# Kernel tuning notes

Measured on AMD Instinct MI355X. Metric: run time of the kernel, lower is better.

Reference implementation:

```python
import jax, jax.numpy as jnp
import numpy as np

B, N, D, H, O = 20000, 32, 128, 256, 128
ATT_SLOPE = 0.01   # nn.LeakyReLU() default inside self.att
ALPHA = 0.2        # leakyrelu slope for attention scores


def _lrelu(v, slope):
    return jnp.where(v > 0, v, slope * v)


def setup_inputs() -> dict:
    key = jax.random.key(0)
    ks = jax.random.split(key, 6)
    x = jax.random.normal(ks[0], (B, D), dtype=jnp.float32)
    neibs = jax.random.normal(ks[1], (B * N, D), dtype=jnp.float32)
    # torch Linear weight is [out,in]; we store transposed [in,out] for x @ W
    W_att = jax.random.normal(ks[2], (D, H), dtype=jnp.float32) / np.sqrt(D)
    W_fcx = jax.random.normal(ks[3], (D, O), dtype=jnp.float32) / np.sqrt(D)
    W_fcn = jax.random.normal(ks[4], (D, O), dtype=jnp.float32) / np.sqrt(D)
    a = jax.random.normal(ks[5], (2 * H, 1), dtype=jnp.float32) * (1.414 * np.sqrt(6.0 / (2 * H + 1)))
    return {"x": x, "neibs": neibs, "W_att": W_att, "W_fcx": W_fcx, "W_fcn": W_fcn, "a": a}


def reference(x, neibs, W_att, W_fcx, W_fcn, a):
    b = x.shape[0]
    n = neibs.shape[0] // b
    # self.att = Linear(no bias) + LeakyReLU(default 0.01)
    x_att = _lrelu(x @ W_att, ATT_SLOPE)                       # [B,H]
    neib_att = _lrelu(neibs @ W_att, ATT_SLOPE).reshape(b, n, -1)  # [B,N,H]
    # cat([x_att.repeat, neib_att]) @ a  ==  x_att @ a[:H] + neib_att @ a[H:]
    h = W_att.shape[1]
    e = _lrelu(x_att @ a[:h, 0] + neib_att @ a[h:, 0][..., None] if False else
               (x_att @ a[:h, 0])[:, None] + jnp.einsum('bnh,h->bn', neib_att, a[h:, 0]), ALPHA)  # [B,N]
    attention = jax.nn.softmax(e, axis=1)                      # softmax over neighbors
    # dropout skipped (eval mode / training=False)
    agg_neib = jnp.einsum('bnd,bn->bd', neibs.reshape(b, n, -1), attention)  # [B,D]
    out = jnp.concatenate([x @ W_fcx, agg_neib @ W_fcn], axis=1)  # combine_fn = cat dim=1
    out = jax.nn.relu(out)                                     # activation
    return out
```

## Files before the change

### kernel.cpp

```cpp
#include <hip/hip_runtime.h>
#include <hip/hip_bf16.h>


#define BB 20000
#define NN 32
#define DD 128
#define HH 256
#define OO 128
#define MB 4
#define ROWS 144
#define AG0 132

typedef __bf16 bf16x8 __attribute__((ext_vector_type(8)));
typedef __bf16 bf16x4 __attribute__((ext_vector_type(4)));
typedef float f32x4 __attribute__((ext_vector_type(4)));

template<int CTRL>
__device__ __forceinline__ float dpp_add(float v) {
    int r = __builtin_amdgcn_update_dpp(0, __builtin_bit_cast(int, v), CTRL, 0xF, 0xF, true);
    return v + __builtin_bit_cast(float, r);
}
__device__ __forceinline__ float red16(float v) {
    v = dpp_add<0x111>(v);
    v = dpp_add<0x112>(v);
    v = dpp_add<0x114>(v);
    v = dpp_add<0x118>(v);
    return v;
}

__global__ void prep_weights(const float* __restrict__ Watt,
                             const float* __restrict__ Wfcx,
                             const float* __restrict__ Wfcn,
                             __bf16* __restrict__ WaT,
                             __bf16* __restrict__ WcT) {
    int idx = blockIdx.x * 256 + threadIdx.x;
    int half = idx >> 15;
    int j = idx & 32767;
    int c = j >> 7, k = j & 127;
    if (half == 0) {
        WaT[j] = (__bf16)Watt[k * HH + c];
    } else {
        float wv = (c < OO) ? Wfcx[k * OO + c] : Wfcn[k * OO + (c - OO)];
        WcT[j] = (__bf16)wv;
    }
}

__launch_bounds__(256, 4)
__global__ void gat_fused(const float* __restrict__ x,
                          const float* __restrict__ neibs,
                          const float* __restrict__ a,
                          const __bf16* __restrict__ WaT,
                          const __bf16* __restrict__ WcT,
                          float* __restrict__ out) {
    __shared__ __bf16 rowsS[ROWS * 128];
    __shared__ float e_part[4][ROWS];

    const int tid = threadIdx.x;
    const int w   = tid >> 6;
    const int l   = tid & 63;
    const int lr  = l & 15;
    const int lg  = l >> 4;
    const int b0  = blockIdx.x * MB;
    char* rbase = (char*)rowsS;

    const int stbase = (tid >> 5) * 256 + ((8 * (tid & 31)) ^ ((tid >> 5) << 4));
    int abase[4];
#pragma unroll
    for (int ks = 0; ks < 4; ++ks)
        abase[ks] = lr * 256 + ((ks * 64 + lg * 16) ^ ((lr & 7) << 4));

    float4 nv[16], xv;
    {
        const float4* np4 = (const float4*)(neibs + (size_t)b0 * NN * DD);
#pragma unroll
        for (int it = 0; it < 16; ++it) nv[it] = np4[it * 256 + tid];
        if (tid < 128) xv = ((const float4*)(x + (size_t)b0 * DD))[tid];
    }
    float aX[4], aN[4];
#pragma unroll
    for (int c4 = 0; c4 < 4; ++c4) {
        int col = (w * 4 + c4) * 16 + lr;
        aX[c4] = a[col];
        aN[c4] = a[HH + col];
    }
#pragma unroll
    for (int it = 0; it < 16; ++it) {
        bf16x4 s = { (__bf16)nv[it].x, (__bf16)nv[it].y, (__bf16)nv[it].z, (__bf16)nv[it].w };
        *(bf16x4*)(rbase + stbase + it * 2048) = s;
    }
    if (tid < 128) {
        bf16x4 s = { (__bf16)xv.x, (__bf16)xv.y, (__bf16)xv.z, (__bf16)xv.w };
        *(bf16x4*)(rbase + stbase + 32768) = s;
    }

    bf16x8 bw[4][4];
#pragma unroll
    for (int c4 = 0; c4 < 4; ++c4)
#pragma unroll
        for (int ks = 0; ks < 4; ++ks)
            bw[c4][ks] = *(const bf16x8*)(WaT + ((w * 4 + c4) * 16 + lr) * 128 + ks * 32 + lg * 8);

    __syncthreads();

#pragma unroll
    for (int rt = 0; rt < 9; ++rt) {
        f32x4 acc[4];
#pragma unroll
        for (int c4 = 0; c4 < 4; ++c4) acc[c4] = (f32x4){0.f, 0.f, 0.f, 0.f};
#pragma unroll
        for (int ks = 0; ks < 4; ++ks) {
            bf16x8 af = *(const bf16x8*)(rbase + abase[ks] + rt * 4096);
#pragma unroll
            for (int c4 = 0; c4 < 4; ++c4)
                acc[c4] = __builtin_amdgcn_mfma_f32_16x16x32_bf16(af, bw[c4][ks], acc[c4], 0, 0, 0);
        }
        float ep[4] = {0.f, 0.f, 0.f, 0.f};
#pragma unroll
        for (int c4 = 0; c4 < 4; ++c4) {
            float av = (rt == 8) ? aX[c4] : aN[c4];
#pragma unroll
            for (int i = 0; i < 4; ++i) {
                float v = acc[c4][i];
                float lv = fmaxf(v, 0.f) + 0.01f * fminf(v, 0.f);
                ep[i] = fmaf(lv, av, ep[i]);
            }
        }
#pragma unroll
        for (int i = 0; i < 4; ++i) ep[i] = red16(ep[i]);
        if (lr == 15) {
            f32x4 st = { ep[0], ep[1], ep[2], ep[3] };
            *(f32x4*)((char*)&e_part[w][0] + rt * 64 + lg * 16) = st;
        }
    }
    __syncthreads();

    float att;
    {
        const int nl = l & 31;
        const int idx = w * 32 + nl;
        float sn = e_part[0][idx] + e_part[1][idx] + e_part[2][idx] + e_part[3][idx];
        const int xr = 128 + w;
        float sx = e_part[0][xr] + e_part[1][xr] + e_part[2][xr] + e_part[3][xr];
        float e = sx + sn;
        e = (e > 0.f) ? e : 0.2f * e;
        float mx = e;
#pragma unroll
        for (int m = 16; m >= 1; m >>= 1) mx = fmaxf(mx, __shfl_xor(mx, m, 32));
        float ex = __expf(e - mx);
        float sum = ex;
#pragma unroll
        for (int m = 16; m >= 1; m >>= 1) sum += __shfl_xor(sum, m, 32);
        att = ex / sum;
    }

    bf16x8 bff[4][4];
#pragma unroll
    for (int c4 = 0; c4 < 4; ++c4)
#pragma unroll
        for (int ks = 0; ks < 4; ++ks)
            bff[c4][ks] = *(const bf16x8*)(WcT + ((w * 4 + c4) * 16 + lr) * 128 + ks * 32 + lg * 8);

    {
        const int half = l >> 5, li = l & 31;
        const int agbase = w * 8192 + 256 * half + ((8 * li) ^ (half << 4));
        float ag[4] = {0.f, 0.f, 0.f, 0.f};
#pragma unroll
        for (int i = 0; i < 16; ++i) {
            float wv = __shfl(att, 2 * i + half, 64);
            bf16x4 v = *(const bf16x4*)(rbase + (agbase ^ ((2 * i & 7) << 4)) + 512 * i);
#pragma unroll
            for (int j = 0; j < 4; ++j) ag[j] = fmaf(wv, (float)v[j], ag[j]);
        }
#pragma unroll
        for (int j = 0; j < 4; ++j) ag[j] += __shfl_xor(ag[j], 32);
        if (half == 0) {
            int row = AG0 + w;
            int off = row * 256 + ((8 * li) ^ ((row & 7) << 4));
            bf16x4 s = { (__bf16)ag[0], (__bf16)ag[1], (__bf16)ag[2], (__bf16)ag[3] };
            *(bf16x4*)(rbase + off) = s;
        }
    }
    __syncthreads();

    {
        f32x4 acc[4];
#pragma unroll
        for (int c4 = 0; c4 < 4; ++c4) acc[c4] = (f32x4){0.f, 0.f, 0.f, 0.f};
#pragma unroll
        for (int ks = 0; ks < 4; ++ks) {
            bf16x8 af = *(const bf16x8*)(rbase + abase[ks] + 32768);
#pragma unroll
            for (int c4 = 0; c4 < 4; ++c4)
                acc[c4] = __builtin_amdgcn_mfma_f32_16x16x32_bf16(af, bff[c4][ks], acc[c4], 0, 0, 0);
        }
#pragma unroll
        for (int c4 = 0; c4 < 4; ++c4) {
            int col = (w * 4 + c4) * 16 + lr;
#pragma unroll
            for (int reg = 0; reg < 4; ++reg) {
                int i = lg * 4 + reg;
                bool doit = (col < 128) ? (i < 4) : (i >= 4 && i < 8);
                if (doit) {
                    float v = fmaxf(acc[c4][reg], 0.f);
                    out[(size_t)(b0 + (i & 3)) * 256 + col] = v;
                }
            }
        }
    }
}

extern "C" void kernel_launch(void* const* d_in, const int* in_sizes, int n_in,
                              void* d_out, int out_size, void* d_ws, size_t ws_size,
                              hipStream_t stream) {
    const float* x    = (const float*)d_in[0];
    const float* nb   = (const float*)d_in[1];
    const float* Watt = (const float*)d_in[2];
    const float* Wfcx = (const float*)d_in[3];
    const float* Wfcn = (const float*)d_in[4];
    const float* a    = (const float*)d_in[5];
    __bf16* WaT = (__bf16*)d_ws;
    __bf16* WcT = WaT + 128 * 256;
    float* o = (float*)d_out;

    prep_weights<<<256, 256, 0, stream>>>(Watt, Wfcx, Wfcn, WaT, WcT);
    gat_fused<<<BB / MB, 256, 0, stream>>>(x, nb, a, WaT, WcT, o);
}
```

Before: 139.3 us.

## Split fused GAT block across 8 waves with fewer columns per wave

Doubles the block to 512 threads, so each wave owns 2 column tiles instead of 4. This halves the per-thread neighbour loads and weight registers and is meant to raise occupancy and latency hiding. The x-row tile is pulled out of the row-tile loop, which is no longer unrolled, and partial attention scores are stored in bf16. Aggregation is restructured so each lane handles one feature with a scalar loop over 32 neighbours. Storing scores in bf16 costs precision, and the scalar aggregation loop issues more LDS loads and shuffles.

```diff
diff --git a/kernel.cpp b/kernel.cpp
--- a/kernel.cpp
+++ b/kernel.cpp
@@ -45,7 +45,7 @@
     }
 }
 
-__launch_bounds__(256, 4)
+__launch_bounds__(512, 6)
 __global__ void gat_fused(const float* __restrict__ x,
                           const float* __restrict__ neibs,
                           const float* __restrict__ a,
@@ -53,7 +53,7 @@
                           const __bf16* __restrict__ WcT,
                           float* __restrict__ out) {
     __shared__ __bf16 rowsS[ROWS * 128];
-    __shared__ float e_part[4][ROWS];
+    __shared__ __bf16 e_part[8][ROWS];
 
     const int tid = threadIdx.x;
     const int w   = tid >> 6;
@@ -63,85 +63,117 @@
     const int b0  = blockIdx.x * MB;
     char* rbase = (char*)rowsS;
 
-    const int stbase = (tid >> 5) * 256 + ((8 * (tid & 31)) ^ ((tid >> 5) << 4));
+    const int s = tid >> 5;
+    const int stbase = s * 256 + ((8 * (tid & 31)) ^ ((s & 7) << 4));
     int abase[4];
 #pragma unroll
     for (int ks = 0; ks < 4; ++ks)
         abase[ks] = lr * 256 + ((ks * 64 + lg * 16) ^ ((lr & 7) << 4));
 
-    float4 nv[16], xv;
+    float4 nv[8], xv;
     {
         const float4* np4 = (const float4*)(neibs + (size_t)b0 * NN * DD);
 #pragma unroll
-        for (int it = 0; it < 16; ++it) nv[it] = np4[it * 256 + tid];
+        for (int it = 0; it < 8; ++it) nv[it] = np4[it * 512 + tid];
         if (tid < 128) xv = ((const float4*)(x + (size_t)b0 * DD))[tid];
     }
-    float aX[4], aN[4];
-#pragma unroll
-    for (int c4 = 0; c4 < 4; ++c4) {
-        int col = (w * 4 + c4) * 16 + lr;
+    float aX[2], aN[2];
+#pragma unroll
+    for (int c4 = 0; c4 < 2; ++c4) {
+        int col = (w * 2 + c4) * 16 + lr;
         aX[c4] = a[col];
         aN[c4] = a[HH + col];
     }
 #pragma unroll
-    for (int it = 0; it < 16; ++it) {
-        bf16x4 s = { (__bf16)nv[it].x, (__bf16)nv[it].y, (__bf16)nv[it].z, (__bf16)nv[it].w };
-        *(bf16x4*)(rbase + stbase + it * 2048) = s;
+    for (int it = 0; it < 8; ++it) {
+        bf16x4 sv = { (__bf16)nv[it].x, (__bf16)nv[it].y, (__bf16)nv[it].z, (__bf16)nv[it].w };
+        *(bf16x4*)(rbase + stbase + it * 4096) = sv;
     }
     if (tid < 128) {
-        bf16x4 s = { (__bf16)xv.x, (__bf16)xv.y, (__bf16)xv.z, (__bf16)xv.w };
-        *(bf16x4*)(rbase + stbase + 32768) = s;
-    }
-
-    bf16x8 bw[4][4];
-#pragma unroll
-    for (int c4 = 0; c4 < 4; ++c4)
-#pragma unroll
-        for (int ks = 0; ks < 4; ++ks)
-            bw[c4][ks] = *(const bf16x8*)(WaT + ((w * 4 + c4) * 16 + lr) * 128 + ks * 32 + lg * 8);
+        bf16x4 sv = { (__bf16)xv.x, (__bf16)xv.y, (__bf16)xv.z, (__bf16)xv.w };
+        *(bf16x4*)(rbase + stbase + 32768) = sv;
+    }
+
+    bf16x8 bw[2][4];
+#pragma unroll
+    for (int c4 = 0; c4 < 2; ++c4)
+#pragma unroll
+        for (int ks = 0; ks < 4; ++ks)
+            bw[c4][ks] = *(const bf16x8*)(WaT + ((w * 2 + c4) * 16 + lr) * 128 + ks * 32 + lg * 8);
 
     __syncthreads();
 
-#pragma unroll
-    for (int rt = 0; rt < 9; ++rt) {
-        f32x4 acc[4];
-#pragma unroll
-        for (int c4 = 0; c4 < 4; ++c4) acc[c4] = (f32x4){0.f, 0.f, 0.f, 0.f};
-#pragma unroll
-        for (int ks = 0; ks < 4; ++ks) {
-            bf16x8 af = *(const bf16x8*)(rbase + abase[ks] + rt * 4096);
-#pragma unroll
-            for (int c4 = 0; c4 < 4; ++c4)
-                acc[c4] = __builtin_amdgcn_mfma_f32_16x16x32_bf16(af, bw[c4][ks], acc[c4], 0, 0, 0);
-        }
+#pragma unroll 1
+    for (int rt = 0; rt < 8; ++rt) {
+        bf16x8 af[4];
+#pragma unroll
+        for (int ks = 0; ks < 4; ++ks)
+            af[ks] = *(const bf16x8*)(rbase + abase[ks] + rt * 4096);
+        f32x4 acc[2];
+#pragma unroll
+        for (int c4 = 0; c4 < 2; ++c4) acc[c4] = (f32x4){0.f, 0.f, 0.f, 0.f};
+#pragma unroll
+        for (int ks = 0; ks < 4; ++ks)
+#pragma unroll
+            for (int c4 = 0; c4 < 2; ++c4)
+                acc[c4] = __builtin_amdgcn_mfma_f32_16x16x32_bf16(af[ks], bw[c4][ks], acc[c4], 0, 0, 0);
         float ep[4] = {0.f, 0.f, 0.f, 0.f};
 #pragma unroll
-        for (int c4 = 0; c4 < 4; ++c4) {
-            float av = (rt == 8) ? aX[c4] : aN[c4];
+        for (int c4 = 0; c4 < 2; ++c4)
 #pragma unroll
             for (int i = 0; i < 4; ++i) {
                 float v = acc[c4][i];
                 float lv = fmaxf(v, 0.f) + 0.01f * fminf(v, 0.f);
-                ep[i] = fmaf(lv, av, ep[i]);
+                ep[i] = fmaf(lv, aN[c4], ep[i]);
             }
-        }
 #pragma unroll
         for (int i = 0; i < 4; ++i) ep[i] = red16(ep[i]);
         if (lr == 15) {
-            f32x4 st = { ep[0], ep[1], ep[2], ep[3] };
-            *(f32x4*)((char*)&e_part[w][0] + rt * 64 + lg * 16) = st;
+            bf16x4 st = { (__bf16)ep[0], (__bf16)ep[1], (__bf16)ep[2], (__bf16)ep[3] };
+            *(bf16x4*)((char*)e_part + w * (2 * ROWS) + rt * 32 + lg * 8) = st;
+        }
+    }
+    {
+        bf16x8 af[4];
+#pragma unroll
+        for (int ks = 0; ks < 4; ++ks)
+            af[ks] = *(const bf16x8*)(rbase + abase[ks] + 32768);
+        f32x4 acc[2];
+#pragma unroll
+        for (int c4 = 0; c4 < 2; ++c4) acc[c4] = (f32x4){0.f, 0.f, 0.f, 0.f};
+#pragma unroll
+        for (int ks = 0; ks < 4; ++ks)
+#pragma unroll
+            for (int c4 = 0; c4 < 2; ++c4)
+                acc[c4] = __builtin_amdgcn_mfma_f32_16x16x32_bf16(af[ks], bw[c4][ks], acc[c4], 0, 0, 0);
+        float ep[4] = {0.f, 0.f, 0.f, 0.f};
+#pragma unroll
+        for (int c4 = 0; c4 < 2; ++c4)
+#pragma unroll
+            for (int i = 0; i < 4; ++i) {
+                float v = acc[c4][i];
+                float lv = fmaxf(v, 0.f) + 0.01f * fminf(v, 0.f);
+                ep[i] = fmaf(lv, aX[c4], ep[i]);
+            }
+#pragma unroll
+        for (int i = 0; i < 4; ++i) ep[i] = red16(ep[i]);
+        if (lr == 15) {
+            bf16x4 st = { (__bf16)ep[0], (__bf16)ep[1], (__bf16)ep[2], (__bf16)ep[3] };
+            *(bf16x4*)((char*)e_part + w * (2 * ROWS) + 256 + lg * 8) = st;
         }
     }
     __syncthreads();
 
+    const int node = w & 3;
     float att;
     {
         const int nl = l & 31;
-        const int idx = w * 32 + nl;
-        float sn = e_part[0][idx] + e_part[1][idx] + e_part[2][idx] + e_part[3][idx];
-        const int xr = 128 + w;
-        float sx = e_part[0][xr] + e_part[1][xr] + e_part[2][xr] + e_part[3][xr];
-        float e = sx + sn;
+        const int idx = node * 32 + nl;
+        const int xr = 128 + node;
+        float e = 0.f;
+#pragma unroll
+        for (int wv = 0; wv < 8; ++wv)
+            e += (float)e_part[wv][idx] + (float)e_part[wv][xr];
         e = (e > 0.f) ? e : 0.2f * e;
         float mx = e;
 #pragma unroll
@@ -153,49 +185,45 @@
         att = ex / sum;
     }
 
-    bf16x8 bff[4][4];
-#pragma unroll
-    for (int c4 = 0; c4 < 4; ++c4)
-#pragma unroll
-        for (int ks = 0; ks < 4; ++ks)
-            bff[c4][ks] = *(const bf16x8*)(WcT + ((w * 4 + c4) * 16 + lr) * 128 + ks * 32 + lg * 8);
-
-    {
-        const int half = l >> 5, li = l & 31;
-        const int agbase = w * 8192 + 256 * half + ((8 * li) ^ (half << 4));
-        float ag[4] = {0.f, 0.f, 0.f, 0.f};
-#pragma unroll
-        for (int i = 0; i < 16; ++i) {
-            float wv = __shfl(att, 2 * i + half, 64);
-            bf16x4 v = *(const bf16x4*)(rbase + (agbase ^ ((2 * i & 7) << 4)) + 512 * i);
-#pragma unroll
-            for (int j = 0; j < 4; ++j) ag[j] = fmaf(wv, (float)v[j], ag[j]);
-        }
-#pragma unroll
-        for (int j = 0; j < 4; ++j) ag[j] += __shfl_xor(ag[j], 32);
-        if (half == 0) {
-            int row = AG0 + w;
-            int off = row * 256 + ((8 * li) ^ ((row & 7) << 4));
-            bf16x4 s = { (__bf16)ag[0], (__bf16)ag[1], (__bf16)ag[2], (__bf16)ag[3] };
-            *(bf16x4*)(rbase + off) = s;
-        }
+    bf16x8 bff[2][4];
+#pragma unroll
+    for (int c4 = 0; c4 < 2; ++c4)
+#pragma unroll
+        for (int ks = 0; ks < 4; ++ks)
+            bff[c4][ks] = *(const bf16x8*)(WcT + ((w * 2 + c4) * 16 + lr) * 128 + ks * 32 + lg * 8);
+
+    {
+        const int d = ((w >> 2) << 6) + l;
+        const int agb = node * 8192 + 2 * d;
+        float ag = 0.f;
+#pragma unroll
+        for (int n = 0; n < 32; ++n) {
+            float wv = __shfl(att, n);
+            __bf16 v = *(const __bf16*)(rbase + (((agb + n * 256)) ^ ((n & 7) << 4)));
+            ag = fmaf(wv, (float)v, ag);
+        }
+        int row = AG0 + node;
+        int off = row * 256 + ((2 * d) ^ ((row & 7) << 4));
+        *(__bf16*)(rbase + off) = (__bf16)ag;
     }
     __syncthreads();
 
     {
-        f32x4 acc[4];
-#pragma unroll
-        for (int c4 = 0; c4 < 4; ++c4) acc[c4] = (f32x4){0.f, 0.f, 0.f, 0.f};
-#pragma unroll
-        for (int ks = 0; ks < 4; ++ks) {
-            bf16x8 af = *(const bf16x8*)(rbase + abase[ks] + 32768);
-#pragma unroll
-            for (int c4 = 0; c4 < 4; ++c4)
-                acc[c4] = __builtin_amdgcn_mfma_f32_16x16x32_bf16(af, bff[c4][ks], acc[c4], 0, 0, 0);
-        }
-#pragma unroll
-        for (int c4 = 0; c4 < 4; ++c4) {
-            int col = (w * 4 + c4) * 16 + lr;
+        bf16x8 af[4];
+#pragma unroll
+        for (int ks = 0; ks < 4; ++ks)
+            af[ks] = *(const bf16x8*)(rbase + abase[ks] + 32768);
+        f32x4 acc[2];
+#pragma unroll
+        for (int c4 = 0; c4 < 2; ++c4) acc[c4] = (f32x4){0.f, 0.f, 0.f, 0.f};
+#pragma unroll
+        for (int ks = 0; ks < 4; ++ks)
+#pragma unroll
+            for (int c4 = 0; c4 < 2; ++c4)
+                acc[c4] = __builtin_amdgcn_mfma_f32_16x16x32_bf16(af[ks], bff[c4][ks], acc[c4], 0, 0, 0);
+#pragma unroll
+        for (int c4 = 0; c4 < 2; ++c4) {
+            int col = (w * 2 + c4) * 16 + lr;
 #pragma unroll
             for (int reg = 0; reg < 4; ++reg) {
                 int i = lg * 4 + reg;
@@ -223,5 +251,5 @@
     float* o = (float*)d_out;
 
     prep_weights<<<256, 256, 0, stream>>>(Watt, Wfcx, Wfcn, WaT, WcT);
-    gat_fused<<<BB / MB, 256, 0, stream>>>(x, nb, a, WaT, WcT, o);
-}
+    gat_fused<<<BB / MB, 512, 0, stream>>>(x, nb, a, WaT, WcT, o);
+}
```

New measurement: 132.1 us. -5.2%, faster.

## Stream neighbor rows into LDS as fp32 via global_load_lds with two batches per block

Applied to the files above, without the earlier changes.

Neighbor rows are now copied straight from global memory into LDS in fp32 with swizzled global_load_lds, instead of passing through registers and being converted to bf16 before the store. The block size drops from 4 to 2 batch items, doubling the grid and reducing the MFMA row tiles. The fp32-to-bf16 conversion moves to the fragment reads, and aggregation reads fp32 directly, with one lane per feature. The aim is to cut register pressure and staging latency, at the cost of twice as many blocks and more redundant per-block weight loads.

```diff
diff --git a/kernel.cpp b/kernel.cpp
--- a/kernel.cpp
+++ b/kernel.cpp
@@ -7,9 +7,7 @@
 #define DD 128
 #define HH 256
 #define OO 128
-#define MB 4
-#define ROWS 144
-#define AG0 132
+#define MB 2
 
 typedef __bf16 bf16x8 __attribute__((ext_vector_type(8)));
 typedef __bf16 bf16x4 __attribute__((ext_vector_type(4)));
@@ -52,72 +50,84 @@
                           const __bf16* __restrict__ WaT,
                           const __bf16* __restrict__ WcT,
                           float* __restrict__ out) {
-    __shared__ __bf16 rowsS[ROWS * 128];
-    __shared__ float e_part[4][ROWS];
+    __shared__ float  nb32[64 * 128];
+    __shared__ __bf16 xagg[16 * 128];
+    __shared__ float  e_part[4][80];
 
     const int tid = threadIdx.x;
     const int w   = tid >> 6;
     const int l   = tid & 63;
     const int lr  = l & 15;
     const int lg  = l >> 4;
+    const int q   = w >> 1;
+    const int dh  = w & 1;
     const int b0  = blockIdx.x * MB;
-    char* rbase = (char*)rowsS;
-
-    const int stbase = (tid >> 5) * 256 + ((8 * (tid & 31)) ^ ((tid >> 5) << 4));
-    int abase[4];
-#pragma unroll
-    for (int ks = 0; ks < 4; ++ks)
-        abase[ks] = lr * 256 + ((ks * 64 + lg * 16) ^ ((lr & 7) << 4));
-
-    float4 nv[16], xv;
-    {
-        const float4* np4 = (const float4*)(neibs + (size_t)b0 * NN * DD);
-#pragma unroll
-        for (int it = 0; it < 16; ++it) nv[it] = np4[it * 256 + tid];
-        if (tid < 128) xv = ((const float4*)(x + (size_t)b0 * DD))[tid];
-    }
+    char* nb = (char*)nb32;
+    char* xb = (char*)xagg;
+
+    {
+        const char* gbase = (const char*)neibs + (size_t)b0 * NN * DD * 4;
+        const int cb = 16 * (l & 31);
+#pragma unroll
+        for (int j = 0; j < 8; ++j) {
+            const int rl  = w * 16 + 2 * j + (l >> 5);
+            const int src = rl * 512 + (cb ^ (((2 * j + (l >> 5)) & 15) << 5));
+            __builtin_amdgcn_global_load_lds(
+                (const __attribute__((address_space(1))) void*)(gbase + src),
+                (__attribute__((address_space(3))) void*)(nb + w * 8192 + j * 1024),
+                16, 0, 0);
+        }
+    }
+    if (tid < 64) {
+        f32x4 v = *((const f32x4*)(x + (size_t)b0 * DD) + tid);
+        int row = tid >> 5, c2 = 8 * (tid & 31);
+        bf16x4 s = { (__bf16)v.x, (__bf16)v.y, (__bf16)v.z, (__bf16)v.w };
+        *(bf16x4*)(xb + row * 256 + (c2 ^ ((row & 7) << 4))) = s;
+    }
+
+    bf16x8 bw[4][4];
     float aX[4], aN[4];
 #pragma unroll
     for (int c4 = 0; c4 < 4; ++c4) {
-        int col = (w * 4 + c4) * 16 + lr;
+        int col = w * 64 + c4 * 16 + lr;
+#pragma unroll
+        for (int ks = 0; ks < 4; ++ks)
+            bw[c4][ks] = *(const bf16x8*)(WaT + (size_t)col * 128 + ks * 32 + lg * 8);
         aX[c4] = a[col];
         aN[c4] = a[HH + col];
     }
-#pragma unroll
-    for (int it = 0; it < 16; ++it) {
-        bf16x4 s = { (__bf16)nv[it].x, (__bf16)nv[it].y, (__bf16)nv[it].z, (__bf16)nv[it].w };
-        *(bf16x4*)(rbase + stbase + it * 2048) = s;
-    }
-    if (tid < 128) {
-        bf16x4 s = { (__bf16)xv.x, (__bf16)xv.y, (__bf16)xv.z, (__bf16)xv.w };
-        *(bf16x4*)(rbase + stbase + 32768) = s;
-    }
-
-    bf16x8 bw[4][4];
-#pragma unroll
-    for (int c4 = 0; c4 < 4; ++c4)
-#pragma unroll
-        for (int ks = 0; ks < 4; ++ks)
-            bw[c4][ks] = *(const bf16x8*)(WaT + ((w * 4 + c4) * 16 + lr) * 128 + ks * 32 + lg * 8);
-
     __syncthreads();
 
 #pragma unroll
-    for (int rt = 0; rt < 9; ++rt) {
+    for (int rt = 0; rt < 5; ++rt) {
+        bf16x8 af[4];
+        if (rt < 4) {
+#pragma unroll
+            for (int ks = 0; ks < 4; ++ks) {
+                const int row = rt * 16 + lr;
+                const char* p = nb + row * 512 + ((ks * 128 + lg * 32) ^ (lr << 5));
+                f32x4 u = *(const f32x4*)p;
+                f32x4 v = *(const f32x4*)(p + 16);
+                af[ks] = (bf16x8){ (__bf16)u.x, (__bf16)u.y, (__bf16)u.z, (__bf16)u.w,
+                                   (__bf16)v.x, (__bf16)v.y, (__bf16)v.z, (__bf16)v.w };
+            }
+        } else {
+#pragma unroll
+            for (int ks = 0; ks < 4; ++ks)
+                af[ks] = *(const bf16x8*)(xb + lr * 256 + ((ks * 64 + lg * 16) ^ ((lr & 7) << 4)));
+        }
         f32x4 acc[4];
 #pragma unroll
         for (int c4 = 0; c4 < 4; ++c4) acc[c4] = (f32x4){0.f, 0.f, 0.f, 0.f};
 #pragma unroll
-        for (int ks = 0; ks < 4; ++ks) {
-            bf16x8 af = *(const bf16x8*)(rbase + abase[ks] + rt * 4096);
+        for (int ks = 0; ks < 4; ++ks)
 #pragma unroll
             for (int c4 = 0; c4 < 4; ++c4)
-                acc[c4] = __builtin_amdgcn_mfma_f32_16x16x32_bf16(af, bw[c4][ks], acc[c4], 0, 0, 0);
-        }
+                acc[c4] = __builtin_amdgcn_mfma_f32_16x16x32_bf16(af[ks], bw[c4][ks], acc[c4], 0, 0, 0);
         float ep[4] = {0.f, 0.f, 0.f, 0.f};
 #pragma unroll
         for (int c4 = 0; c4 < 4; ++c4) {
-            float av = (rt == 8) ? aX[c4] : aN[c4];
+            float av = (rt == 4) ? aX[c4] : aN[c4];
 #pragma unroll
             for (int i = 0; i < 4; ++i) {
                 float v = acc[c4][i];
@@ -137,11 +147,10 @@
     float att;
     {
         const int nl = l & 31;
-        const int idx = w * 32 + nl;
-        float sn = e_part[0][idx] + e_part[1][idx] + e_part[2][idx] + e_part[3][idx];
-        const int xr = 128 + w;
-        float sx = e_part[0][xr] + e_part[1][xr] + e_part[2][xr] + e_part[3][xr];
-        float e = sx + sn;
+        const int idx = q * 32 + nl;
+        const int xr = 64 + q;
+        float e = e_part[0][idx] + e_part[1][idx] + e_part[2][idx] + e_part[3][idx]
+                + e_part[0][xr]  + e_part[1][xr]  + e_part[2][xr]  + e_part[3][xr];
         e = (e > 0.f) ? e : 0.2f * e;
         float mx = e;
 #pragma unroll
@@ -158,51 +167,55 @@
     for (int c4 = 0; c4 < 4; ++c4)
 #pragma unroll
         for (int ks = 0; ks < 4; ++ks)
-            bff[c4][ks] = *(const bf16x8*)(WcT + ((w * 4 + c4) * 16 + lr) * 128 + ks * 32 + lg * 8);
-
-    {
-        const int half = l >> 5, li = l & 31;
-        const int agbase = w * 8192 + 256 * half + ((8 * li) ^ (half << 4));
-        float ag[4] = {0.f, 0.f, 0.f, 0.f};
-#pragma unroll
-        for (int i = 0; i < 16; ++i) {
-            float wv = __shfl(att, 2 * i + half, 64);
-            bf16x4 v = *(const bf16x4*)(rbase + (agbase ^ ((2 * i & 7) << 4)) + 512 * i);
-#pragma unroll
-            for (int j = 0; j < 4; ++j) ag[j] = fmaf(wv, (float)v[j], ag[j]);
-        }
-#pragma unroll
-        for (int j = 0; j < 4; ++j) ag[j] += __shfl_xor(ag[j], 32);
-        if (half == 0) {
-            int row = AG0 + w;
-            int off = row * 256 + ((8 * li) ^ ((row & 7) << 4));
-            bf16x4 s = { (__bf16)ag[0], (__bf16)ag[1], (__bf16)ag[2], (__bf16)ag[3] };
-            *(bf16x4*)(rbase + off) = s;
-        }
+            bff[c4][ks] = *(const bf16x8*)(WcT + (size_t)(w * 64 + c4 * 16 + lr) * 128 + ks * 32 + lg * 8);
+
+    {
+        const int d = dh * 64 + l;
+        const int dcb = 4 * d;
+        float ag0 = 0.f, ag1 = 0.f, ag2 = 0.f, ag3 = 0.f;
+#pragma unroll
+        for (int n4 = 0; n4 < 8; ++n4) {
+#pragma unroll
+            for (int pp = 0; pp < 4; ++pp) {
+                const int n = n4 * 4 + pp;
+                float wv = __shfl(att, n);
+                const int row = q * 32 + n;
+                float v = *(const float*)(nb + row * 512 + (dcb ^ ((row & 15) << 5)));
+                if (pp == 0) ag0 = fmaf(wv, v, ag0);
+                else if (pp == 1) ag1 = fmaf(wv, v, ag1);
+                else if (pp == 2) ag2 = fmaf(wv, v, ag2);
+                else ag3 = fmaf(wv, v, ag3);
+            }
+        }
+        float ag = (ag0 + ag1) + (ag2 + ag3);
+        const int arow = 2 + q;
+        *(__bf16*)(xb + arow * 256 + ((2 * d) ^ ((arow & 7) << 4))) = (__bf16)ag;
     }
     __syncthreads();
 
     {
+        bf16x8 af[4];
+#pragma unroll
+        for (int ks = 0; ks < 4; ++ks)
+            af[ks] = *(const bf16x8*)(xb + lr * 256 + ((ks * 64 + lg * 16) ^ ((lr & 7) << 4)));
         f32x4 acc[4];
 #pragma unroll
         for (int c4 = 0; c4 < 4; ++c4) acc[c4] = (f32x4){0.f, 0.f, 0.f, 0.f};
 #pragma unroll
-        for (int ks = 0; ks < 4; ++ks) {
-            bf16x8 af = *(const bf16x8*)(rbase + abase[ks] + 32768);
+        for (int ks = 0; ks < 4; ++ks)
 #pragma unroll
             for (int c4 = 0; c4 < 4; ++c4)
-                acc[c4] = __builtin_amdgcn_mfma_f32_16x16x32_bf16(af, bff[c4][ks], acc[c4], 0, 0, 0);
-        }
-#pragma unroll
-        for (int c4 = 0; c4 < 4; ++c4) {
-            int col = (w * 4 + c4) * 16 + lr;
-#pragma unroll
-            for (int reg = 0; reg < 4; ++reg) {
-                int i = lg * 4 + reg;
-                bool doit = (col < 128) ? (i < 4) : (i >= 4 && i < 8);
-                if (doit) {
-                    float v = fmaxf(acc[c4][reg], 0.f);
-                    out[(size_t)(b0 + (i & 3)) * 256 + col] = v;
+                acc[c4] = __builtin_amdgcn_mfma_f32_16x16x32_bf16(af[ks], bff[c4][ks], acc[c4], 0, 0, 0);
+        if (lg == 0) {
+#pragma unroll
+            for (int c4 = 0; c4 < 4; ++c4) {
+                int col = w * 64 + c4 * 16 + lr;
+                if (col < 128) {
+                    out[(size_t)(b0 + 0) * 256 + col] = fmaxf(acc[c4][0], 0.f);
+                    out[(size_t)(b0 + 1) * 256 + col] = fmaxf(acc[c4][1], 0.f);
+                } else {
+                    out[(size_t)(b0 + 0) * 256 + col] = fmaxf(acc[c4][2], 0.f);
+                    out[(size_t)(b0 + 1) * 256 + col] = fmaxf(acc[c4][3], 0.f);
                 }
             }
         }
@@ -219,7 +232,7 @@
     const float* Wfcn = (const float*)d_in[4];
     const float* a    = (const float*)d_in[5];
     __bf16* WaT = (__bf16*)d_ws;
-    __bf16* WcT = WaT + 128 * 256;
+    __bf16* WcT = WaT + 32768;
     float* o = (float*)d_out;
 
     prep_weights<<<256, 256, 0, stream>>>(Watt, Wfcx, Wfcn, WaT, WcT);
```

Measured after the change: 187.0 us. 34.2% more time.
